# Kernel optimization log

Measured on AMD Instinct MI355X. Metric: run time of the kernel, lower is better.

The kernel has to match this reference:

```python
import jax, jax.numpy as jnp
import numpy as np

N, IN_F, OUT_F = 8192, 4096, 4096
QMIN, QMAX = -128, 127  # int8 range for bitwidth 8


def setup_inputs() -> dict:
    key = jax.random.key(0)
    k1, k2, k3, k4 = jax.random.split(key, 4)
    x = jax.random.randint(k1, (N, IN_F), QMIN, QMAX + 1, dtype=jnp.int32).astype(jnp.int8)
    weight = jax.random.randint(k2, (OUT_F, IN_F), QMIN, QMAX + 1, dtype=jnp.int32).astype(jnp.int8)
    bias = jax.random.randint(k3, (OUT_F,), -1024, 1024, dtype=jnp.int32)
    weight_scale = jax.random.uniform(k4, (OUT_F,), dtype=jnp.float32, minval=0.001, maxval=0.02)
    input_scale = jnp.asarray([0.05], dtype=jnp.float32)
    output_scale = jnp.asarray([0.1], dtype=jnp.float32)
    output_zero_point = 0
    return {"x": x, "weight": weight, "bias": bias, "weight_scale": weight_scale,
            "input_scale": input_scale, "output_scale": output_scale,
            "output_zero_point": output_zero_point}


def reference(x, weight, bias, weight_scale, input_scale, output_scale, output_zero_point):
    # int32-accumulated GEMM with bias (CPU path of the torch module)
    acc = jnp.matmul(x.astype(jnp.int32), weight.astype(jnp.int32).T) + bias[None, :]  # [N, OUT_F] int32
    # fused dequant/requant epilogue
    scale_factor = (input_scale * weight_scale / output_scale)[None, :]  # [1, OUT_F]
    out = acc.astype(jnp.float32) * scale_factor + output_zero_point
    out = jnp.clip(jnp.round(out), QMIN, QMAX).astype(jnp.int8)
    return out
```

## Files before the change

kernel.cpp:

```cpp
#include <hip/hip_runtime.h>
#include <stdint.h>


#define M_DIM 8192
#define N_DIM 4096
#define K_DIM 4096
#define BM 256
#define BN 256
#define NKT2 (K_DIM / 32)
#define NT (K_DIM / 64)
#define NBLK ((M_DIM / BM) * (N_DIM / BN))
#define ABUF (BM * 64)
#define BBUF (BN * 64)

using i32x4  = __attribute__((ext_vector_type(4))) int;
using i32x16 = __attribute__((ext_vector_type(16))) int;

typedef const __attribute__((address_space(1))) uint32_t* gptr_t;
typedef __attribute__((address_space(3))) uint32_t* lptr_t;

__device__ __forceinline__ void gload_lds16(const void* g, void* l) {
    __builtin_amdgcn_global_load_lds((gptr_t)g, (lptr_t)l, 16, 0, 0);
}

__device__ __forceinline__ int pack4(i32x4 v) {
    return (int)(((unsigned)v.x & 0xFFu) | (((unsigned)v.y & 0xFFu) << 8) |
                 (((unsigned)v.z & 0xFFu) << 16) | (((unsigned)v.w) << 24));
}

__global__ void pack_panels32_kernel(const int* __restrict__ src, int8_t* __restrict__ dst,
                                     int n_blocks) {
    int gid = blockIdx.x * blockDim.x + threadIdx.x;
    int blk = gid >> 6;
    int l = gid & 63;
    if (blk >= n_blocks) return;
    int rb = blk >> 7;
    int kt = blk & (NKT2 - 1);
    const i32x4* s4 = (const i32x4*)(src + (size_t)(rb * 32 + (l & 31)) * K_DIM
                                         + kt * 32 + (l >> 5) * 16);
    i32x4 o;
    o.x = pack4(s4[0]); o.y = pack4(s4[1]); o.z = pack4(s4[2]); o.w = pack4(s4[3]);
    *(i32x4*)(dst + (size_t)blk * 1024 + l * 16) = o;
}

#define MFMA32(a, b, c) __builtin_amdgcn_mfma_i32_32x32x32_i8((a), (b), (c), 0, 0, 0)

#define FRAG_A(r, k) (*(const i32x4*)(Acur + (r) * 2048 + (k) * 1024))
#define FRAG_B(c, k) (*(const i32x4*)(Bcur + (c) * 2048 + (k) * 1024))

#define PHASEK(k, STAGE_STMTS, TAIL_STMTS)                                        \
  { i32x4 a0 = FRAG_A(0,k), a1 = FRAG_A(1,k), a2 = FRAG_A(2,k), a3 = FRAG_A(3,k); \
    i32x4 b0 = FRAG_B(0,k), b1 = FRAG_B(1,k);                                     \
    STAGE_STMTS;                                                                  \
    __builtin_amdgcn_s_barrier();                                                 \
    asm volatile("s_waitcnt lgkmcnt(0)" ::: "memory");                            \
    __builtin_amdgcn_sched_barrier(0);                                            \
    __builtin_amdgcn_s_setprio(1);                                                \
    acc[0][0] = MFMA32(a0, b0, acc[0][0]); acc[0][1] = MFMA32(a0, b1, acc[0][1]); \
    acc[1][0] = MFMA32(a1, b0, acc[1][0]); acc[1][1] = MFMA32(a1, b1, acc[1][1]); \
    acc[2][0] = MFMA32(a2, b0, acc[2][0]); acc[2][1] = MFMA32(a2, b1, acc[2][1]); \
    acc[3][0] = MFMA32(a3, b0, acc[3][0]); acc[3][1] = MFMA32(a3, b1, acc[3][1]); \
    __builtin_amdgcn_s_setprio(0);                                                \
    TAIL_STMTS;                                                                   \
    __builtin_amdgcn_s_barrier(); }

__global__ __launch_bounds__(512, 2)
void qgemm32_kernel(const int8_t* __restrict__ xp, const int8_t* __restrict__ wp,
                    const int* __restrict__ bias, const float* __restrict__ wscale,
                    const float* __restrict__ iscale, const float* __restrict__ oscale,
                    const int* __restrict__ zp, int* __restrict__ out) {
    extern __shared__ int8_t lds[];
    int8_t* As = lds;
    int8_t* Bs = lds + 3 * ABUF;

    const int tid  = threadIdx.x;
    const int wave = tid >> 6;
    const int lane = tid & 63;

    int b = blockIdx.x;
    int s = (b & 7) * (NBLK >> 3) + (b >> 3);
    const int bcol = (s & 15) * BN;
    const int brow = (s >> 4) * BM;

    const int wr = wave >> 2;
    const int wc = wave & 3;

    const int rb0 = brow >> 5;
    const int cb0 = bcol >> 5;
    const int8_t* AgP = xp + ((size_t)(rb0 + wave) * NKT2) * 1024 + lane * 16;
    const int8_t* BgP = wp + ((size_t)(cb0 + wave) * NKT2) * 1024 + lane * 16;
    const int aoff = wave * 2048;

    i32x16 acc[4][2] = {};

    #pragma unroll
    for (int t0 = 0; t0 < 2; t0++) {
        int8_t* Ad = As + t0 * ABUF;
        int8_t* Bd = Bs + t0 * BBUF;
        gload_lds16(AgP + (size_t)(2 * t0) * 1024,     Ad + aoff);
        gload_lds16(AgP + (size_t)(2 * t0 + 1) * 1024, Ad + aoff + 1024);
        gload_lds16(BgP + (size_t)(2 * t0) * 1024,     Bd + aoff);
        gload_lds16(BgP + (size_t)(2 * t0 + 1) * 1024, Bd + aoff + 1024);
    }
    asm volatile("s_waitcnt vmcnt(4)" ::: "memory");
    __builtin_amdgcn_s_barrier();

    int cur = 0, stg = 2;
    for (int t = 0; t < NT - 2; ++t) {
        const int8_t* Acur = As + cur * ABUF + wr * 8192 + lane * 16;
        const int8_t* Bcur = Bs + cur * BBUF + wc * 4096 + lane * 16;
        int8_t* Astg = As + stg * ABUF;
        int8_t* Bstg = Bs + stg * BBUF;
        const size_t k0 = (size_t)(2 * (t + 2)) * 1024;

        PHASEK(0,
            { gload_lds16(AgP + k0,        Astg + aoff);
              gload_lds16(AgP + k0 + 1024, Astg + aoff + 1024); },
            ((void)0))
        PHASEK(1,
            { gload_lds16(BgP + k0,        Bstg + aoff);
              gload_lds16(BgP + k0 + 1024, Bstg + aoff + 1024); },
            asm volatile("s_waitcnt vmcnt(4)" ::: "memory"))

        cur = (cur == 2) ? 0 : cur + 1;
        stg = (stg == 2) ? 0 : stg + 1;
    }
    {
        const int8_t* Acur = As + cur * ABUF + wr * 8192 + lane * 16;
        const int8_t* Bcur = Bs + cur * BBUF + wc * 4096 + lane * 16;
        PHASEK(0, ((void)0), ((void)0))
        PHASEK(1, ((void)0), asm volatile("s_waitcnt vmcnt(0)" ::: "memory"))
        cur = (cur == 2) ? 0 : cur + 1;
    }
    {
        const int8_t* Acur = As + cur * ABUF + wr * 8192 + lane * 16;
        const int8_t* Bcur = Bs + cur * BBUF + wc * 4096 + lane * 16;
        PHASEK(0, ((void)0), ((void)0))
        PHASEK(1, ((void)0), ((void)0))
    }

    const float is_v = iscale[0];
    const float os_v = oscale[0];
    const float zpf = (float)zp[0];
    #pragma unroll
    for (int c = 0; c < 2; c++) {
        int col = bcol + wc * 64 + c * 32 + (lane & 31);
        float sf = (is_v * wscale[col]) / os_v;
        int bz = bias[col];
        #pragma unroll
        for (int r = 0; r < 4; r++) {
            int rowb = brow + wr * 128 + r * 32 + 4 * (lane >> 5);
            #pragma unroll
            for (int reg = 0; reg < 16; reg++) {
                int row = rowb + (reg & 3) + 8 * (reg >> 2);
                float v = (float)(acc[r][c][reg] + bz) * sf + zpf;
                v = rintf(v);
                v = fminf(fmaxf(v, -128.0f), 127.0f);
                out[(size_t)row * N_DIM + col] = (int)v;
            }
        }
    }
}

#define MFMA_I8(a, b, c) __builtin_amdgcn_mfma_i32_16x16x64_i8((a), (b), (c), 0, 0, 0)

__global__ void qgemm_fallback(const int* __restrict__ x32, const int* __restrict__ w32,
                               const int* __restrict__ bias, const float* __restrict__ wscale,
                               const float* __restrict__ iscale, const float* __restrict__ oscale,
                               const int* __restrict__ zp, int* __restrict__ out) {
    __shared__ int8_t As[128][64];
    __shared__ int8_t Bs[128][64];
    const int tid  = threadIdx.x;
    const int wave = tid >> 6;
    const int lane = tid & 63;
    int b = blockIdx.x;
    int s = (b & 7) * (gridDim.x >> 3) + (b >> 3);
    const int bcol = (s & 31) * 128;
    const int brow = (s >> 5) * 128;
    const int wr = wave >> 1;
    const int wc = wave & 1;
    i32x4 acc[4][4] = {};
    for (int kt = 0; kt < K_DIM; kt += 64) {
        int row = tid >> 1;
        int h = tid & 1;
        const i32x4* sa = (const i32x4*)(x32 + (size_t)(brow + row) * K_DIM + kt + h * 32);
        const i32x4* sb = (const i32x4*)(w32 + (size_t)(bcol + row) * K_DIM + kt + h * 32);
        int pa[8], pb[8];
        #pragma unroll
        for (int j = 0; j < 8; j++) { pa[j] = pack4(sa[j]); pb[j] = pack4(sb[j]); }
        *(i32x4*)&As[row][h * 32]      = *(i32x4*)&pa[0];
        *(i32x4*)&As[row][h * 32 + 16] = *(i32x4*)&pa[4];
        *(i32x4*)&Bs[row][h * 32]      = *(i32x4*)&pb[0];
        *(i32x4*)&Bs[row][h * 32 + 16] = *(i32x4*)&pb[4];
        __syncthreads();
        i32x4 a_frag[4], b_frag[4];
        #pragma unroll
        for (int m = 0; m < 4; m++)
            a_frag[m] = *(const i32x4*)&As[wr * 64 + m * 16 + (lane & 15)][(lane >> 4) * 16];
        #pragma unroll
        for (int n = 0; n < 4; n++)
            b_frag[n] = *(const i32x4*)&Bs[wc * 64 + n * 16 + (lane & 15)][(lane >> 4) * 16];
        #pragma unroll
        for (int m = 0; m < 4; m++)
            #pragma unroll
            for (int n = 0; n < 4; n++)
                acc[m][n] = MFMA_I8(a_frag[m], b_frag[n], acc[m][n]);
        __syncthreads();
    }
    const float is_v = iscale[0];
    const float os_v = oscale[0];
    const float zpf = (float)zp[0];
    #pragma unroll
    for (int n = 0; n < 4; n++) {
        int col = bcol + wc * 64 + n * 16 + (lane & 15);
        float sf = (is_v * wscale[col]) / os_v;
        int bz = bias[col];
        #pragma unroll
        for (int m = 0; m < 4; m++) {
            int row0 = brow + wr * 64 + m * 16 + (lane >> 4) * 4;
            #pragma unroll
            for (int r = 0; r < 4; r++) {
                float v = (float)(acc[m][n][r] + bz) * sf + zpf;
                v = rintf(v);
                v = fminf(fmaxf(v, -128.0f), 127.0f);
                out[(size_t)(row0 + r) * N_DIM + col] = (int)v;
            }
        }
    }
}

extern "C" void kernel_launch(void* const* d_in, const int* in_sizes, int n_in,
                              void* d_out, int out_size, void* d_ws, size_t ws_size,
                              hipStream_t stream) {
    const int*   x32    = (const int*)d_in[0];
    const int*   w32    = (const int*)d_in[1];
    const int*   bias   = (const int*)d_in[2];
    const float* wscale = (const float*)d_in[3];
    const float* iscale = (const float*)d_in[4];
    const float* oscale = (const float*)d_in[5];
    const int*   zp     = (const int*)d_in[6];
    int* out = (int*)d_out;

    const size_t need = (size_t)M_DIM * K_DIM + (size_t)N_DIM * K_DIM;
    const size_t lds_bytes = 3 * (size_t)(ABUF + BBUF);

    if (ws_size >= need) {
        int8_t* xp = (int8_t*)d_ws;
        int8_t* wp = xp + (size_t)M_DIM * K_DIM;
        const int nblkA = (M_DIM / 32) * NKT2;
        const int nblkB = (N_DIM / 32) * NKT2;
        pack_panels32_kernel<<<nblkA / 4, 256, 0, stream>>>(x32, xp, nblkA);
        pack_panels32_kernel<<<nblkB / 4, 256, 0, stream>>>(w32, wp, nblkB);
        (void)hipFuncSetAttribute((const void*)qgemm32_kernel,
                                  hipFuncAttributeMaxDynamicSharedMemorySize,
                                  (int)lds_bytes);
        qgemm32_kernel<<<NBLK, 512, lds_bytes, stream>>>(xp, wp, bias, wscale, iscale, oscale, zp, out);
    } else {
        qgemm_fallback<<<2048, 256, 0, stream>>>(x32, w32, bias, wscale, iscale, oscale, zp, out);
    }
}
```

Before: 187.2 us.

## Restructure int8 GEMM main loop into 4-slot LDS ring with register-prefetched fragments

Replaces the 3-slot LDS ring, which had two barrier pairs per K-tile, with a 4-slot ring that needs one wait and one barrier per tile. LDS fragments for the next tile are double-buffered in registers and read while the current tile's MFMAs issue. The loop is unrolled by four with fixed slot indices, so the per-iteration modulo slot arithmetic goes away. In exchange LDS per block grows to 128KB. The extra fragment registers, on top of the large accumulator set, may cause register pressure or spills under the 512x2 launch bounds.

```diff
diff --git a/kernel.cpp b/kernel.cpp
--- a/kernel.cpp
+++ b/kernel.cpp
@@ -45,24 +45,43 @@
 
 #define MFMA32(a, b, c) __builtin_amdgcn_mfma_i32_32x32x32_i8((a), (b), (c), 0, 0, 0)
 
-#define FRAG_A(r, k) (*(const i32x4*)(Acur + (r) * 2048 + (k) * 1024))
-#define FRAG_B(c, k) (*(const i32x4*)(Bcur + (c) * 2048 + (k) * 1024))
-
-#define PHASEK(k, STAGE_STMTS, TAIL_STMTS)                                        \
-  { i32x4 a0 = FRAG_A(0,k), a1 = FRAG_A(1,k), a2 = FRAG_A(2,k), a3 = FRAG_A(3,k); \
-    i32x4 b0 = FRAG_B(0,k), b1 = FRAG_B(1,k);                                     \
-    STAGE_STMTS;                                                                  \
-    __builtin_amdgcn_s_barrier();                                                 \
-    asm volatile("s_waitcnt lgkmcnt(0)" ::: "memory");                            \
-    __builtin_amdgcn_sched_barrier(0);                                            \
+#define RA(S, R, K) (*(const i32x4*)(Ard + (S) * ABUF + (R) * 2048 + (K) * 1024))
+#define RB(S, C, K) (*(const i32x4*)(Brd + (S) * BBUF + (C) * 2048 + (K) * 1024))
+
+#define READ_HALF(NS, SLOT, K)                                          \
+    fA[NS][K][0] = RA(SLOT, 0, K); fA[NS][K][1] = RA(SLOT, 1, K);       \
+    fA[NS][K][2] = RA(SLOT, 2, K); fA[NS][K][3] = RA(SLOT, 3, K);       \
+    fB[NS][K][0] = RB(SLOT, 0, K); fB[NS][K][1] = RB(SLOT, 1, K);
+
+#define MFMA_HALF(CS, K)                                                          \
     __builtin_amdgcn_s_setprio(1);                                                \
-    acc[0][0] = MFMA32(a0, b0, acc[0][0]); acc[0][1] = MFMA32(a0, b1, acc[0][1]); \
-    acc[1][0] = MFMA32(a1, b0, acc[1][0]); acc[1][1] = MFMA32(a1, b1, acc[1][1]); \
-    acc[2][0] = MFMA32(a2, b0, acc[2][0]); acc[2][1] = MFMA32(a2, b1, acc[2][1]); \
-    acc[3][0] = MFMA32(a3, b0, acc[3][0]); acc[3][1] = MFMA32(a3, b1, acc[3][1]); \
-    __builtin_amdgcn_s_setprio(0);                                                \
-    TAIL_STMTS;                                                                   \
-    __builtin_amdgcn_s_barrier(); }
+    acc[0][0] = MFMA32(fA[CS][K][0], fB[CS][K][0], acc[0][0]);                    \
+    acc[0][1] = MFMA32(fA[CS][K][0], fB[CS][K][1], acc[0][1]);                    \
+    acc[1][0] = MFMA32(fA[CS][K][1], fB[CS][K][0], acc[1][0]);                    \
+    acc[1][1] = MFMA32(fA[CS][K][1], fB[CS][K][1], acc[1][1]);                    \
+    acc[2][0] = MFMA32(fA[CS][K][2], fB[CS][K][0], acc[2][0]);                    \
+    acc[2][1] = MFMA32(fA[CS][K][2], fB[CS][K][1], acc[2][1]);                    \
+    acc[3][0] = MFMA32(fA[CS][K][3], fB[CS][K][0], acc[3][0]);                    \
+    acc[3][1] = MFMA32(fA[CS][K][3], fB[CS][K][1], acc[3][1]);                    \
+    __builtin_amdgcn_s_setprio(0);
+
+#define STAGE(SLOT)                                                     \
+    gload_lds16(AgS,        ldsA + (SLOT) * ABUF + waoff);              \
+    gload_lds16(AgS + 1024, ldsA + (SLOT) * ABUF + waoff + 1024);       \
+    gload_lds16(BgS,        ldsB + (SLOT) * BBUF + waoff);              \
+    gload_lds16(BgS + 1024, ldsB + (SLOT) * BBUF + waoff + 1024);       \
+    AgS += 2048; BgS += 2048;
+
+#define TILE_STEADY(SLOT_STG, SLOT_NXT, CS, NS)                         \
+  { STAGE(SLOT_STG)                                                     \
+    asm volatile("s_waitcnt vmcnt(4)" ::: "memory");                    \
+    __builtin_amdgcn_s_barrier();                                       \
+    READ_HALF(NS, SLOT_NXT, 0)                                          \
+    __builtin_amdgcn_sched_barrier(0);                                  \
+    MFMA_HALF(CS, 0)                                                    \
+    READ_HALF(NS, SLOT_NXT, 1)                                          \
+    __builtin_amdgcn_sched_barrier(0);                                  \
+    MFMA_HALF(CS, 1) }
 
 __global__ __launch_bounds__(512, 2)
 void qgemm32_kernel(const int8_t* __restrict__ xp, const int8_t* __restrict__ wp,
@@ -70,8 +89,8 @@
                     const float* __restrict__ iscale, const float* __restrict__ oscale,
                     const int* __restrict__ zp, int* __restrict__ out) {
     extern __shared__ int8_t lds[];
-    int8_t* As = lds;
-    int8_t* Bs = lds + 3 * ABUF;
+    int8_t* ldsA = lds;
+    int8_t* ldsB = lds + 4 * ABUF;
 
     const int tid  = threadIdx.x;
     const int wave = tid >> 6;
@@ -87,57 +106,44 @@
 
     const int rb0 = brow >> 5;
     const int cb0 = bcol >> 5;
-    const int8_t* AgP = xp + ((size_t)(rb0 + wave) * NKT2) * 1024 + lane * 16;
-    const int8_t* BgP = wp + ((size_t)(cb0 + wave) * NKT2) * 1024 + lane * 16;
-    const int aoff = wave * 2048;
+    const int8_t* AgS = xp + ((size_t)(rb0 + wave) * NKT2) * 1024 + lane * 16;
+    const int8_t* BgS = wp + ((size_t)(cb0 + wave) * NKT2) * 1024 + lane * 16;
+    const int waoff = wave * 2048;
+
+    const int8_t* Ard = ldsA + wr * 8192 + lane * 16;
+    const int8_t* Brd = ldsB + wc * 4096 + lane * 16;
 
     i32x16 acc[4][2] = {};
-
-    #pragma unroll
-    for (int t0 = 0; t0 < 2; t0++) {
-        int8_t* Ad = As + t0 * ABUF;
-        int8_t* Bd = Bs + t0 * BBUF;
-        gload_lds16(AgP + (size_t)(2 * t0) * 1024,     Ad + aoff);
-        gload_lds16(AgP + (size_t)(2 * t0 + 1) * 1024, Ad + aoff + 1024);
-        gload_lds16(BgP + (size_t)(2 * t0) * 1024,     Bd + aoff);
-        gload_lds16(BgP + (size_t)(2 * t0 + 1) * 1024, Bd + aoff + 1024);
-    }
+    i32x4 fA[2][2][4];
+    i32x4 fB[2][2][2];
+
+    STAGE(0)
+    STAGE(1)
     asm volatile("s_waitcnt vmcnt(4)" ::: "memory");
     __builtin_amdgcn_s_barrier();
-
-    int cur = 0, stg = 2;
-    for (int t = 0; t < NT - 2; ++t) {
-        const int8_t* Acur = As + cur * ABUF + wr * 8192 + lane * 16;
-        const int8_t* Bcur = Bs + cur * BBUF + wc * 4096 + lane * 16;
-        int8_t* Astg = As + stg * ABUF;
-        int8_t* Bstg = Bs + stg * BBUF;
-        const size_t k0 = (size_t)(2 * (t + 2)) * 1024;
-
-        PHASEK(0,
-            { gload_lds16(AgP + k0,        Astg + aoff);
-              gload_lds16(AgP + k0 + 1024, Astg + aoff + 1024); },
-            ((void)0))
-        PHASEK(1,
-            { gload_lds16(BgP + k0,        Bstg + aoff);
-              gload_lds16(BgP + k0 + 1024, Bstg + aoff + 1024); },
-            asm volatile("s_waitcnt vmcnt(4)" ::: "memory"))
-
-        cur = (cur == 2) ? 0 : cur + 1;
-        stg = (stg == 2) ? 0 : stg + 1;
-    }
+    READ_HALF(0, 0, 0)
+    READ_HALF(0, 0, 1)
+
+    for (int i = 0; i < 15; ++i) {
+        TILE_STEADY(2, 1, 0, 1)
+        TILE_STEADY(3, 2, 1, 0)
+        TILE_STEADY(0, 3, 0, 1)
+        TILE_STEADY(1, 0, 1, 0)
+    }
+    TILE_STEADY(2, 1, 0, 1)
+    TILE_STEADY(3, 2, 1, 0)
     {
-        const int8_t* Acur = As + cur * ABUF + wr * 8192 + lane * 16;
-        const int8_t* Bcur = Bs + cur * BBUF + wc * 4096 + lane * 16;
-        PHASEK(0, ((void)0), ((void)0))
-        PHASEK(1, ((void)0), asm volatile("s_waitcnt vmcnt(0)" ::: "memory"))
-        cur = (cur == 2) ? 0 : cur + 1;
-    }
-    {
-        const int8_t* Acur = As + cur * ABUF + wr * 8192 + lane * 16;
-        const int8_t* Bcur = Bs + cur * BBUF + wc * 4096 + lane * 16;
-        PHASEK(0, ((void)0), ((void)0))
-        PHASEK(1, ((void)0), ((void)0))
-    }
+        asm volatile("s_waitcnt vmcnt(0)" ::: "memory");
+        __builtin_amdgcn_s_barrier();
+        READ_HALF(1, 3, 0)
+        __builtin_amdgcn_sched_barrier(0);
+        MFMA_HALF(0, 0)
+        READ_HALF(1, 3, 1)
+        __builtin_amdgcn_sched_barrier(0);
+        MFMA_HALF(0, 1)
+    }
+    MFMA_HALF(1, 0)
+    MFMA_HALF(1, 1)
 
     const float is_v = iscale[0];
     const float os_v = oscale[0];
@@ -242,7 +248,7 @@
     int* out = (int*)d_out;
 
     const size_t need = (size_t)M_DIM * K_DIM + (size_t)N_DIM * K_DIM;
-    const size_t lds_bytes = 3 * (size_t)(ABUF + BBUF);
+    const size_t lds_bytes = 4 * (size_t)(ABUF + BBUF);
 
     if (ws_size >= need) {
         int8_t* xp = (int8_t*)d_ws;
```

Result: faster. 182.3 us (-2.6%).
